# Kernel tuning notes

Hardware: AMD Instinct MI355X
Metric: run time of the kernel (lower is better)

The kernel has to match this reference:

```python
import jax, jax.numpy as jnp
import numpy as np

GROUP_SIZE = 64

def _dequant_w4(qweight, wscales):
    """Unpack int4 weights and apply per-(group, out-channel) scales.
    qweight: [N, K//2] uint8-valued ints, low nibble = even k, high nibble = odd k.
    wscales: [K//GROUP_SIZE, N] float. Returns [N, K] float weight.
    """
    q = qweight.astype(jnp.int32)
    low = (q & 15) - 8          # [N, K//2], signed int4
    high = ((q >> 4) & 15) - 8  # [N, K//2]
    N = q.shape[0]
    K = q.shape[1] * 2
    w_int = jnp.stack([low, high], axis=-1).reshape(N, K)  # interleaved low/high
    # scale[n, k] = wscales[k // GROUP_SIZE, n]
    scale = jnp.repeat(wscales, GROUP_SIZE, axis=0).T  # [N, K]
    return w_int.astype(wscales.dtype) * scale

def setup_inputs() -> dict:
    key = jax.random.key(0)
    ks = jax.random.split(key, 7)
    M, K, N, R = 8192, 4096, 4096, 32
    x = jax.random.normal(ks[0], (M, K), dtype=jnp.float32)
    qweight = jax.random.randint(ks[1], (N, K // 2), 0, 256, dtype=jnp.int32)
    wscales = jax.random.uniform(ks[2], (K // GROUP_SIZE, N), dtype=jnp.float32) * 0.01 + 0.001
    proj_down = jax.random.normal(ks[3], (R, K), dtype=jnp.float32) * 0.02
    proj_up = jax.random.normal(ks[4], (N, R), dtype=jnp.float32) * 0.02
    wtscale = jnp.ones((1,), dtype=jnp.float32)
    bias = jax.random.normal(ks[5], (N,), dtype=jnp.float32) * 0.01
    return {"x": x, "qweight": qweight, "wscales": wscales,
            "proj_down": proj_down, "proj_up": proj_up,
            "wtscale": wtscale, "bias": bias}

def reference(x, qweight, wscales, proj_down, proj_up, wtscale, bias):
    # Dequant int4 weight, GEMM, low-rank LoRA correction scaled by wtscale, bias.
    w = _dequant_w4(qweight, wscales)              # [N, K]
    out = x @ w.T                                  # [M, N]
    lora = (x @ proj_down.T) @ proj_up.T           # [M, R] @ [R, N] -> [M, N]
    out = out + lora * wtscale
    out = out + bias
    return out
```

## Files before the change

### kernel.cpp

```cpp
#include <hip/hip_runtime.h>
#include <hip/hip_bf16.h>
#include <stdint.h>

#define MD 8192
#define ND 4096
#define KD 4096
#define RD 32

typedef __bf16 bf16x8 __attribute__((ext_vector_type(8)));
typedef float f32x4 __attribute__((ext_vector_type(4)));

__device__ __forceinline__ void cp16(const void* g, void* l) {
    __builtin_amdgcn_global_load_lds(
        (const __attribute__((address_space(1))) void*)g,
        (__attribute__((address_space(3))) void*)l, 16, 0, 0);
}

__global__ __launch_bounds__(256) void cvt_x(const float* __restrict__ x,
                                             __hip_bfloat16* __restrict__ y) {
    size_t i = ((size_t)blockIdx.x * 256 + threadIdx.x) * 8;
    float4 a = *(const float4*)(x + i);
    float4 b = *(const float4*)(x + i + 4);
    union { __hip_bfloat16 h[8]; uint4 u; } o;
    o.h[0] = __float2bfloat16(a.x); o.h[1] = __float2bfloat16(a.y);
    o.h[2] = __float2bfloat16(a.z); o.h[3] = __float2bfloat16(a.w);
    o.h[4] = __float2bfloat16(b.x); o.h[5] = __float2bfloat16(b.y);
    o.h[6] = __float2bfloat16(b.z); o.h[7] = __float2bfloat16(b.w);
    *(uint4*)(y + i) = o.u;
}

__global__ __launch_bounds__(256) void build_weff(
    const int* __restrict__ qw,
    const float* __restrict__ wsc,
    const float* __restrict__ pd,
    const float* __restrict__ pu,
    const float* __restrict__ wts_p,
    __hip_bfloat16* __restrict__ weff)
{
    __shared__ float pd_s[RD][132];
    __shared__ float pu_t[RD][68];
    const int t = threadIdx.x;
    const int kb = blockIdx.x * 128;
    const int nb = blockIdx.y * 64;

    for (int f = t; f < (RD * 128) / 4; f += 256) {
        int r = f >> 5;
        int c = (f & 31) << 2;
        *(float4*)&pd_s[r][c] = *(const float4*)(pd + (size_t)r * KD + kb + c);
    }
    for (int f = t; f < (64 * RD) / 4; f += 256) {
        int nl = f >> 3;
        int r4 = (f & 7) << 2;
        float4 v = *(const float4*)(pu + (size_t)(nb + nl) * RD + r4);
        pu_t[r4 + 0][nl] = v.x; pu_t[r4 + 1][nl] = v.y;
        pu_t[r4 + 2][nl] = v.z; pu_t[r4 + 3][nl] = v.w;
    }
    __syncthreads();

    const float wts = wts_p[0];
    const int kc = (t & 15) << 3;
    const int ng = (t >> 4) << 2;

    float acc[4][8];
#pragma unroll
    for (int i = 0; i < 4; ++i)
#pragma unroll
        for (int j = 0; j < 8; ++j) acc[i][j] = 0.f;

    for (int r = 0; r < RD; ++r) {
        float4 pda = *(const float4*)&pd_s[r][kc];
        float4 pdb = *(const float4*)&pd_s[r][kc + 4];
        float4 puv = *(const float4*)&pu_t[r][ng];
        float pus[4] = {puv.x, puv.y, puv.z, puv.w};
        float pdv[8] = {pda.x, pda.y, pda.z, pda.w, pdb.x, pdb.y, pdb.z, pdb.w};
#pragma unroll
        for (int i = 0; i < 4; ++i)
#pragma unroll
            for (int j = 0; j < 8; ++j)
                acc[i][j] += pus[i] * pdv[j];
    }

    const int kg = kb + kc;
    const int g = kg >> 6;
#pragma unroll
    for (int i = 0; i < 4; ++i) {
        const int n = nb + ng + i;
        const float sc = wsc[(size_t)g * ND + n];
        int4 q = *(const int4*)(qw + (size_t)n * (KD / 2) + (kg >> 1));
        const int qi[4] = {q.x, q.y, q.z, q.w};
        union { __hip_bfloat16 h[8]; uint4 u; } o;
#pragma unroll
        for (int j = 0; j < 4; ++j) {
            const int lo = (qi[j] & 15) - 8;
            const int hi = ((qi[j] >> 4) & 15) - 8;
            o.h[2 * j]     = __float2bfloat16((float)lo * sc + wts * acc[i][2 * j]);
            o.h[2 * j + 1] = __float2bfloat16((float)hi * sc + wts * acc[i][2 * j + 1]);
        }
        *(uint4*)(weff + (size_t)n * KD + kg) = o.u;
    }
}

__global__ __launch_bounds__(256) void gemm_bt_bias(
    const __hip_bfloat16* __restrict__ A,
    const __hip_bfloat16* __restrict__ B,
    const float* __restrict__ bias,
    float* __restrict__ C)
{
    __shared__ alignas(16) __hip_bfloat16 As[128 * 64];
    __shared__ alignas(16) __hip_bfloat16 Bs[128 * 64];

    const int t = threadIdx.x;
    const int lane = t & 63;
    const int wave = t >> 6;
    const int wr = wave >> 1;
    const int wc = wave & 1;

    const int bid = blockIdx.x;
    const int nb = (bid & 7) * 4 + ((bid >> 3) & 3);
    const int mb = bid >> 5;
    const int m0 = mb * 128;
    const int n0 = nb * 128;

    const int srow = t >> 3;
    const int gchunk = (t & 7) ^ ((t >> 3) & 7);
    const __hip_bfloat16* Ag = A + (size_t)(m0 + srow) * KD + gchunk * 8;
    const __hip_bfloat16* Bg = B + (size_t)(n0 + srow) * KD + gchunk * 8;
    char* AsB = (char*)As + wave * 1024;
    char* BsB = (char*)Bs + wave * 1024;

    const int qm = lane & 15;
    const int c = lane >> 4;
    const int sl0 = ((c) ^ (qm & 7)) * 8;
    const int sl1 = ((4 + c) ^ (qm & 7)) * 8;

    f32x4 acc[4][4];
#pragma unroll
    for (int i = 0; i < 4; ++i)
#pragma unroll
        for (int j = 0; j < 4; ++j) acc[i][j] = (f32x4){0.f, 0.f, 0.f, 0.f};

    for (int kt = 0; kt < KD; kt += 64) {
#pragma unroll
        for (int p = 0; p < 4; ++p) {
            cp16(Ag + kt + (size_t)p * 32 * KD, AsB + p * 4096);
            cp16(Bg + kt + (size_t)p * 32 * KD, BsB + p * 4096);
        }
        __syncthreads();

        bf16x8 af[4][2], bfr[4][2];
#pragma unroll
        for (int i = 0; i < 4; ++i) {
            const int row = (wr * 64 + i * 16 + qm) * 64;
            af[i][0] = *(const bf16x8*)(As + row + sl0);
            af[i][1] = *(const bf16x8*)(As + row + sl1);
        }
#pragma unroll
        for (int j = 0; j < 4; ++j) {
            const int row = (wc * 64 + j * 16 + qm) * 64;
            bfr[j][0] = *(const bf16x8*)(Bs + row + sl0);
            bfr[j][1] = *(const bf16x8*)(Bs + row + sl1);
        }

#pragma unroll
        for (int i = 0; i < 4; ++i)
#pragma unroll
            for (int j = 0; j < 4; ++j)
                acc[i][j] = __builtin_amdgcn_mfma_f32_16x16x32_bf16(
                    af[i][0], bfr[j][0], acc[i][j], 0, 0, 0);
#pragma unroll
        for (int i = 0; i < 4; ++i)
#pragma unroll
            for (int j = 0; j < 4; ++j)
                acc[i][j] = __builtin_amdgcn_mfma_f32_16x16x32_bf16(
                    af[i][1], bfr[j][1], acc[i][j], 0, 0, 0);
        __syncthreads();
    }

    const int cm0 = (lane >> 4) * 4;
    const int cn = lane & 15;
#pragma unroll
    for (int j = 0; j < 4; ++j) {
        const int n = n0 + wc * 64 + j * 16 + cn;
        const float bv = bias[n];
#pragma unroll
        for (int i = 0; i < 4; ++i) {
            const int mr = m0 + wr * 64 + i * 16 + cm0;
            float* dst = C + (size_t)mr * ND + n;
#pragma unroll
            for (int r = 0; r < 4; ++r)
                dst[(size_t)r * ND] = acc[i][j][r] + bv;
        }
    }
}

extern "C" void kernel_launch(void* const* d_in, const int* in_sizes, int n_in,
                              void* d_out, int out_size, void* d_ws, size_t ws_size,
                              hipStream_t stream) {
    const float* x    = (const float*)d_in[0];
    const int* qw     = (const int*)d_in[1];
    const float* wsc  = (const float*)d_in[2];
    const float* pd   = (const float*)d_in[3];
    const float* pu   = (const float*)d_in[4];
    const float* wts  = (const float*)d_in[5];
    const float* bias = (const float*)d_in[6];
    float* out = (float*)d_out;

    __hip_bfloat16* weff = (__hip_bfloat16*)d_ws;
    __hip_bfloat16* xbf  = (__hip_bfloat16*)((char*)d_ws + (size_t)ND * KD * sizeof(__hip_bfloat16));

    cvt_x<<<(MD * (size_t)KD) / (256 * 8), 256, 0, stream>>>(x, xbf);
    build_weff<<<dim3(KD / 128, ND / 64), 256, 0, stream>>>(qw, wsc, pd, pu, wts, weff);
    gemm_bt_bias<<<2048, 256, 0, stream>>>(xbf, weff, bias, out);
}
```

Before: 523.9 us.

## Rewrite GEMM as 256x256 tile, 8-wave, double-buffered LDS pipeline

Result: slower. 588.4 us (+12.3%).

```diff
diff --git a/kernel.cpp b/kernel.cpp
--- a/kernel.cpp
+++ b/kernel.cpp
@@ -100,92 +100,138 @@
     }
 }
 
-__global__ __launch_bounds__(256) void gemm_bt_bias(
+#define FENCE asm volatile("" ::: "memory")
+#define VMW4 asm volatile("s_waitcnt vmcnt(4)" ::: "memory")
+#define VMW2 asm volatile("s_waitcnt vmcnt(2)" ::: "memory")
+#define VMW0 asm volatile("s_waitcnt vmcnt(0)" ::: "memory")
+#define VMNONE
+#define ENDB __builtin_amdgcn_s_barrier(); FENCE
+#define ENDNONE
+
+#define PHASE(QI, QJ, CB, STAGE, WAITM, ENDM)                                  \
+    {                                                                          \
+        bf16x8 af[4][2], bfr[2][2];                                            \
+        const char* Ab = ArowBase + (CB) + (QI) * 8192;                        \
+        const char* Bb = BrowBase + (CB) + (QJ) * 4096;                        \
+        _Pragma("unroll") for (int i = 0; i < 4; ++i) {                        \
+            af[i][0] = *(const bf16x8*)(Ab + i * 2048 + slh0);                 \
+            af[i][1] = *(const bf16x8*)(Ab + i * 2048 + slh1);                 \
+        }                                                                      \
+        _Pragma("unroll") for (int j = 0; j < 2; ++j) {                        \
+            bfr[j][0] = *(const bf16x8*)(Bb + j * 2048 + slh0);                \
+            bfr[j][1] = *(const bf16x8*)(Bb + j * 2048 + slh1);               \
+        }                                                                      \
+        STAGE;                                                                 \
+        WAITM;                                                                 \
+        __builtin_amdgcn_s_barrier();                                          \
+        asm volatile("s_waitcnt lgkmcnt(0)" ::: "memory");                     \
+        __builtin_amdgcn_sched_barrier(0);                                     \
+        __builtin_amdgcn_s_setprio(1);                                         \
+        _Pragma("unroll") for (int i = 0; i < 4; ++i)                          \
+            _Pragma("unroll") for (int j = 0; j < 2; ++j) {                    \
+                acc[(QI) * 4 + i][(QJ) * 2 + j] =                              \
+                    __builtin_amdgcn_mfma_f32_16x16x32_bf16(                   \
+                        af[i][0], bfr[j][0], acc[(QI) * 4 + i][(QJ) * 2 + j],  \
+                        0, 0, 0);                                              \
+                acc[(QI) * 4 + i][(QJ) * 2 + j] =                              \
+                    __builtin_amdgcn_mfma_f32_16x16x32_bf16(                   \
+                        af[i][1], bfr[j][1], acc[(QI) * 4 + i][(QJ) * 2 + j],  \
+                        0, 0, 0);                                              \
+            }                                                                  \
+        __builtin_amdgcn_s_setprio(0);                                         \
+        ENDM;                                                                  \
+    }
+
+__global__ __launch_bounds__(512, 2) void gemm_bt_bias(
     const __hip_bfloat16* __restrict__ A,
     const __hip_bfloat16* __restrict__ B,
     const float* __restrict__ bias,
     float* __restrict__ C)
 {
-    __shared__ alignas(16) __hip_bfloat16 As[128 * 64];
-    __shared__ alignas(16) __hip_bfloat16 Bs[128 * 64];
+    __shared__ alignas(16) char As[2][32768];
+    __shared__ alignas(16) char Bs[2][32768];
 
     const int t = threadIdx.x;
     const int lane = t & 63;
-    const int wave = t >> 6;
-    const int wr = wave >> 1;
-    const int wc = wave & 1;
+    const int w = t >> 6;
+    const int wm = w >> 2;
+    const int wn = w & 3;
 
     const int bid = blockIdx.x;
-    const int nb = (bid & 7) * 4 + ((bid >> 3) & 3);
-    const int mb = bid >> 5;
-    const int m0 = mb * 128;
-    const int n0 = nb * 128;
-
-    const int srow = t >> 3;
-    const int gchunk = (t & 7) ^ ((t >> 3) & 7);
-    const __hip_bfloat16* Ag = A + (size_t)(m0 + srow) * KD + gchunk * 8;
-    const __hip_bfloat16* Bg = B + (size_t)(n0 + srow) * KD + gchunk * 8;
-    char* AsB = (char*)As + wave * 1024;
-    char* BsB = (char*)Bs + wave * 1024;
+    const int swz = (bid & 7) * 64 + (bid >> 3);
+    const int m0 = (swz >> 4) * 256;
+    const int n0 = (swz & 15) * 256;
+
+    const int lrow = lane >> 3;
+    const int gch = (lane & 7) ^ lrow;
+    const __hip_bfloat16* Ag = A + (size_t)(m0 + lrow) * KD + gch * 8;
+    const __hip_bfloat16* Bg = B + (size_t)(n0 + lrow) * KD + gch * 8;
+
+    const int a1 = w, a2 = 16 + w, a3 = 8 + w, a4 = 24 + w;
+    const int bq = wm * 8 + wn;
+    const int b1 = bq, b2 = bq + 16, b3 = bq + 4, b4 = bq + 20;
 
     const int qm = lane & 15;
-    const int c = lane >> 4;
-    const int sl0 = ((c) ^ (qm & 7)) * 8;
-    const int sl1 = ((4 + c) ^ (qm & 7)) * 8;
-
-    f32x4 acc[4][4];
-#pragma unroll
-    for (int i = 0; i < 4; ++i)
+    const int c4 = lane >> 4;
+    const int slh0 = (c4 ^ (qm & 7)) * 16;
+    const int slh1 = ((4 + c4) ^ (qm & 7)) * 16;
+    const char* ArowBase = (const char*)As + (wm * 128 + qm) * 128;
+    const char* BrowBase = (const char*)Bs + (wn * 64 + qm) * 128;
+
+    cp16(Ag + (size_t)a1 * 8 * KD, (char*)As + a1 * 1024);
+    cp16(Ag + (size_t)a2 * 8 * KD, (char*)As + a2 * 1024);
+    cp16(Bg + (size_t)b1 * 8 * KD, (char*)Bs + b1 * 1024);
+    cp16(Bg + (size_t)b2 * 8 * KD, (char*)Bs + b2 * 1024);
+    cp16(Ag + (size_t)a3 * 8 * KD, (char*)As + a3 * 1024);
+    cp16(Ag + (size_t)a4 * 8 * KD, (char*)As + a4 * 1024);
+    cp16(Bg + (size_t)b3 * 8 * KD, (char*)Bs + b3 * 1024);
+    cp16(Bg + (size_t)b4 * 8 * KD, (char*)Bs + b4 * 1024);
+
+    f32x4 acc[8][4];
+#pragma unroll
+    for (int i = 0; i < 8; ++i)
 #pragma unroll
         for (int j = 0; j < 4; ++j) acc[i][j] = (f32x4){0.f, 0.f, 0.f, 0.f};
 
-    for (int kt = 0; kt < KD; kt += 64) {
-#pragma unroll
-        for (int p = 0; p < 4; ++p) {
-            cp16(Ag + kt + (size_t)p * 32 * KD, AsB + p * 4096);
-            cp16(Bg + kt + (size_t)p * 32 * KD, BsB + p * 4096);
-        }
-        __syncthreads();
-
-        bf16x8 af[4][2], bfr[4][2];
-#pragma unroll
-        for (int i = 0; i < 4; ++i) {
-            const int row = (wr * 64 + i * 16 + qm) * 64;
-            af[i][0] = *(const bf16x8*)(As + row + sl0);
-            af[i][1] = *(const bf16x8*)(As + row + sl1);
-        }
-#pragma unroll
-        for (int j = 0; j < 4; ++j) {
-            const int row = (wc * 64 + j * 16 + qm) * 64;
-            bfr[j][0] = *(const bf16x8*)(Bs + row + sl0);
-            bfr[j][1] = *(const bf16x8*)(Bs + row + sl1);
-        }
-
-#pragma unroll
-        for (int i = 0; i < 4; ++i)
-#pragma unroll
-            for (int j = 0; j < 4; ++j)
-                acc[i][j] = __builtin_amdgcn_mfma_f32_16x16x32_bf16(
-                    af[i][0], bfr[j][0], acc[i][j], 0, 0, 0);
-#pragma unroll
-        for (int i = 0; i < 4; ++i)
-#pragma unroll
-            for (int j = 0; j < 4; ++j)
-                acc[i][j] = __builtin_amdgcn_mfma_f32_16x16x32_bf16(
-                    af[i][1], bfr[j][1], acc[i][j], 0, 0, 0);
-        __syncthreads();
-    }
-
-    const int cm0 = (lane >> 4) * 4;
+    VMW4;
+    __builtin_amdgcn_s_barrier();
+    FENCE;
+
+    for (int kt = 0; kt < 63; ++kt) {
+        const int cb = (kt & 1) << 15;
+        const int sb = cb ^ 32768;
+        const size_t ko = (size_t)(kt + 1) * 64;
+        PHASE(0, 0, cb,
+              (cp16(Ag + (size_t)a1 * 8 * KD + ko, (char*)As + sb + a1 * 1024),
+               cp16(Ag + (size_t)a2 * 8 * KD + ko, (char*)As + sb + a2 * 1024)),
+              VMW4, ENDB)
+        PHASE(1, 0, cb,
+              (cp16(Bg + (size_t)b1 * 8 * KD + ko, (char*)Bs + sb + b1 * 1024),
+               cp16(Bg + (size_t)b2 * 8 * KD + ko, (char*)Bs + sb + b2 * 1024)),
+              VMW4, ENDB)
+        PHASE(0, 1, cb,
+              (cp16(Ag + (size_t)a3 * 8 * KD + ko, (char*)As + sb + a3 * 1024),
+               cp16(Ag + (size_t)a4 * 8 * KD + ko, (char*)As + sb + a4 * 1024)),
+              VMNONE, ENDB)
+        PHASE(1, 1, cb,
+              (cp16(Bg + (size_t)b3 * 8 * KD + ko, (char*)Bs + sb + b3 * 1024),
+               cp16(Bg + (size_t)b4 * 8 * KD + ko, (char*)Bs + sb + b4 * 1024)),
+              VMW4, ENDB)
+    }
+    PHASE(0, 0, 32768, ((void)0), VMW2, ENDB)
+    PHASE(1, 0, 32768, ((void)0), VMW0, ENDB)
+    PHASE(0, 1, 32768, ((void)0), VMNONE, ENDB)
+    PHASE(1, 1, 32768, ((void)0), VMNONE, ENDNONE)
+
+    const int cm = (lane >> 4) << 2;
     const int cn = lane & 15;
 #pragma unroll
     for (int j = 0; j < 4; ++j) {
-        const int n = n0 + wc * 64 + j * 16 + cn;
+        const int n = n0 + wn * 64 + j * 16 + cn;
         const float bv = bias[n];
 #pragma unroll
-        for (int i = 0; i < 4; ++i) {
-            const int mr = m0 + wr * 64 + i * 16 + cm0;
-            float* dst = C + (size_t)mr * ND + n;
+        for (int i = 0; i < 8; ++i) {
+            float* dst = C + (size_t)(m0 + wm * 128 + i * 16 + cm) * ND + n;
 #pragma unroll
             for (int r = 0; r < 4; ++r)
                 dst[(size_t)r * ND] = acc[i][j][r] + bv;
@@ -210,5 +256,5 @@
 
     cvt_x<<<(MD * (size_t)KD) / (256 * 8), 256, 0, stream>>>(x, xbf);
     build_weff<<<dim3(KD / 128, ND / 64), 256, 0, stream>>>(qw, wsc, pd, pu, wts, weff);
-    gemm_bt_bias<<<2048, 256, 0, stream>>>(xbf, weff, bias, out);
-}
+    gemm_bt_bias<<<512, 512, 0, stream>>>(xbf, weff, bias, out);
+}
```
